# Kernel optimization log

Hardware: AMD Instinct MI355X
Metric: run time of the kernel (lower is better)

Reference implementation:

```python
import jax, jax.numpy as jnp
import numpy as np

B, CIN, COUT, L, K, HEADS, GROUPS, EPS = 16, 256, 512, 1024, 3, 8, 32, 1e-5


def group_norm(x, w, b, groups, eps=EPS):
    Bx, C, Lx = x.shape
    g = x.reshape(Bx, groups, C // groups, Lx)
    mu = g.mean(axis=(2, 3), keepdims=True)
    var = g.var(axis=(2, 3), keepdims=True)
    g = (g - mu) * jax.lax.rsqrt(var + eps)
    return g.reshape(Bx, C, Lx) * w[None, :, None] + b[None, :, None]


def conv1d(x, w, b, pad):
    y = jax.lax.conv_general_dilated(x, w, window_strides=(1,), padding=[(pad, pad)],
                                     dimension_numbers=('NCH', 'OIH', 'NCH'))
    return y + b[None, :, None]


def setup_inputs() -> dict:
    key = jax.random.key(0)
    ks = jax.random.split(key, 12)
    def kn(k, shape, fan_in, scale=1.0):
        return (np.sqrt(1.0 / fan_in) * jax.random.normal(k, shape, dtype=jnp.float32)) * scale
    return {
        'x': jax.random.normal(ks[0], (B, CIN, L), dtype=jnp.float32),
        'norm0_w': jnp.ones((CIN,), jnp.float32), 'norm0_b': jnp.zeros((CIN,), jnp.float32),
        'conv0_w': kn(ks[1], (COUT, CIN, K), CIN * K), 'conv0_b': jnp.zeros((COUT,), jnp.float32),
        'norm1_w': jnp.ones((COUT,), jnp.float32), 'norm1_b': jnp.zeros((COUT,), jnp.float32),
        'conv1_w': kn(ks[2], (COUT, COUT, K), COUT * K, 1e-5), 'conv1_b': jnp.zeros((COUT,), jnp.float32),
        'skip_w': kn(ks[3], (COUT, CIN, 1), CIN), 'skip_b': jnp.zeros((COUT,), jnp.float32),
        'norm2_w': jnp.ones((COUT,), jnp.float32), 'norm2_b': jnp.zeros((COUT,), jnp.float32),
        'qkv_w': kn(ks[4], (COUT * 3, COUT, 1), COUT), 'qkv_b': jnp.zeros((COUT * 3,), jnp.float32),
        'proj_w': kn(ks[5], (COUT, COUT, 1), COUT, 1e-5), 'proj_b': jnp.zeros((COUT,), jnp.float32),
    }


def reference(x, norm0_w, norm0_b, conv0_w, conv0_b, norm1_w, norm1_b, conv1_w, conv1_b,
              skip_w, skip_b, norm2_w, norm2_b, qkv_w, qkv_b, proj_w, proj_b):
    orig = x
    h = conv1d(jax.nn.silu(group_norm(x, norm0_w, norm0_b, min(GROUPS, CIN))), conv0_w, conv0_b, (K - 1) // 2)
    h = jax.nn.silu(group_norm(h, norm1_w, norm1_b, min(GROUPS, COUT)))
    h = conv1d(h, conv1_w, conv1_b, (K - 1) // 2)
    h = h + conv1d(orig, skip_w, skip_b, 0)  # skip (in != out), dropout p=0
    # skip_scale = 1
    # attention: qkv [B, 3C, L] -> [B*H, C/H, 3, L] (channel axis splits as H, C/H, 3)
    qkv = conv1d(group_norm(h, norm2_w, norm2_b, min(GROUPS, COUT)), qkv_w, qkv_b, 0)
    ch = COUT // HEADS
    qkv = qkv.reshape(B * HEADS, ch, 3, L)
    q, k, v = qkv[:, :, 0], qkv[:, :, 1], qkv[:, :, 2]  # each [BH, ch, L]
    scores = jnp.einsum('nci,ncj->nij', q, k) / np.sqrt(ch).astype(np.float32)
    attn = jax.nn.softmax(scores, axis=-1)
    a = jnp.einsum('nij,ncj->nci', attn, v).reshape(B, COUT, L)
    return h + conv1d(a, proj_w, proj_b, 0)
```

## Files before the change

### kernel.cpp

```cpp
#include <hip/hip_runtime.h>


typedef float f32x4 __attribute__((ext_vector_type(4)));
typedef float f32x16 __attribute__((ext_vector_type(16)));
typedef short short8 __attribute__((ext_vector_type(8)));

__device__ __forceinline__ unsigned short f2bf(float f) {
  union { float f; unsigned u; } v; v.f = f;
  return (unsigned short)((v.u + 0x7FFFu + ((v.u >> 16) & 1u)) >> 16);
}

__device__ __forceinline__ void gload_lds16(const void* g, void* l) {
  __builtin_amdgcn_global_load_lds(
      (const __attribute__((address_space(1))) unsigned int*)g,
      (__attribute__((address_space(3))) unsigned int*)l, 16, 0, 0);
}

__device__ __forceinline__ float swap_add(float x) {
  float a = x, b = x;
  asm("v_permlane32_swap_b32 %0, %1" : "+v"(a), "+v"(b));
  return a + b;
}

__device__ __forceinline__ short8 pack8(float a0, float a1, float a2, float a3,
                                        float a4, float a5, float a6, float a7) {
  unsigned x0, x1, x2, x3;
  asm("v_cvt_pk_bf16_f32 %0, %1, %2" : "=v"(x0) : "v"(a0), "v"(a1));
  asm("v_cvt_pk_bf16_f32 %0, %1, %2" : "=v"(x1) : "v"(a2), "v"(a3));
  asm("v_cvt_pk_bf16_f32 %0, %1, %2" : "=v"(x2) : "v"(a4), "v"(a5));
  asm("v_cvt_pk_bf16_f32 %0, %1, %2" : "=v"(x3) : "v"(a6), "v"(a7));
  asm("v_permlane32_swap_b32 %0, %1" : "+v"(x0), "+v"(x2));
  asm("v_permlane32_swap_b32 %0, %1" : "+v"(x1), "+v"(x3));
  union { unsigned u[4]; short8 s; } r;
  r.u[0] = x0; r.u[1] = x1; r.u[2] = x2; r.u[3] = x3;
  return r.s;
}
#define PACK8(V, B) pack8(V[B+0], V[B+1], V[B+2], V[B+3], V[B+4], V[B+5], V[B+6], V[B+7])

template<int CPG>
__global__ __launch_bounds__(256) void gn_stats_kernel(
    const float* __restrict__ in, float2* __restrict__ mr,
    unsigned short* __restrict__ outT) {
  constexpr int C = CPG * 32;
  constexpr int N = CPG * 1024;
  const int g = blockIdx.x & 31;
  const int bb = blockIdx.x >> 5;
  const size_t base = ((size_t)bb * C + g * CPG) * 1024;
  const int t = threadIdx.x;
  float s = 0.f, ss = 0.f;
#pragma unroll
  for (int i = t * 4; i < N; i += 1024) {
    const float4 v = *(const float4*)(in + base + i);
    s += (v.x + v.y) + (v.z + v.w);
    ss += (v.x * v.x + v.y * v.y) + (v.z * v.z + v.w * v.w);
  }
#pragma unroll
  for (int off = 32; off; off >>= 1) {
    s += __shfl_down(s, off);
    ss += __shfl_down(ss, off);
  }
  __shared__ float2 red[4];
  if ((t & 63) == 0) red[t >> 6] = make_float2(s, ss);
  __syncthreads();
  const float2 r0 = red[0], r1 = red[1], r2 = red[2], r3 = red[3];
  const float tots = (r0.x + r1.x) + (r2.x + r3.x);
  const float totss = (r0.y + r1.y) + (r2.y + r3.y);
  constexpr float inv_n = 1.0f / (float)N;
  const float mean = tots * inv_n;
  const float var = totss * inv_n - mean * mean;
  const float rstd = rsqrtf(var + 1e-5f);
  if (t == 0) mr[bb * 32 + g] = make_float2(mean, rstd);
  unsigned short* ob = outT + (size_t)bb * 1026 * C + g * CPG;
  if (t < CPG) {
    ob[t] = 0;
    ob[(size_t)1025 * C + t] = 0;
  }
}

template<int MODE, bool SILU, int C, bool PADZ>
__global__ __launch_bounds__(256) void nt_kernel(
    const float* __restrict__ in, const float2* __restrict__ st,
    const float* __restrict__ gw, const float* __restrict__ gb,
    unsigned short* __restrict__ outT) {
  constexpr int CPG = C / 32;
  __shared__ float ls[64][65];
  __shared__ float2 gstat[4];
  const int b = blockIdx.z, c0 = blockIdx.y * 64, l0 = blockIdx.x * 64;
  const int t = threadIdx.x;
  if (MODE == 2) {
    if (t < 4) {
      const int g = (c0 >> 4) + t;
      const float2* p = st + (((size_t)b * 4 + (g >> 3)) * 8 + (g & 7)) * 8;
      float s = 0.f, ss = 0.f;
#pragma unroll
      for (int i = 0; i < 8; ++i) { s += p[i].x; ss += p[i].y; }
      const float mean = s * (1.f / 16384.f);
      const float var = ss * (1.f / 16384.f) - mean * mean;
      gstat[t] = make_float2(mean, rsqrtf(var + 1e-5f));
    }
    __syncthreads();
  }
  const int lw = (t & 15) * 4;
  const int cr = t >> 4;
#pragma unroll
  for (int p = 0; p < 4; ++p) {
    const int c = p * 16 + cr;
    const int cc = c0 + c;
    float sc = 1.f, bi = 0.f;
    if (MODE == 1) {
      const float2 ms = st[b * 32 + cc / CPG];
      sc = gw[cc] * ms.y;
      bi = gb[cc] - ms.x * sc;
    } else if (MODE == 2) {
      const float2 ms = gstat[c >> 4];
      sc = gw[cc] * ms.y;
      bi = gb[cc] - ms.x * sc;
    }
    const float4 v = *(const float4*)(in + ((size_t)b * C + cc) * 1024 + l0 + lw);
    float o[4] = {v.x * sc + bi, v.y * sc + bi, v.z * sc + bi, v.w * sc + bi};
    if (SILU) {
#pragma unroll
      for (int d = 0; d < 4; ++d) o[d] = o[d] / (1.f + __expf(-o[d]));
    }
#pragma unroll
    for (int d = 0; d < 4; ++d) ls[c][lw + d] = o[d];
  }
  __syncthreads();
  const int l = t >> 2, c16 = (t & 3) * 16;
  short8 v0, v1;
#pragma unroll
  for (int j = 0; j < 8; ++j) v0[j] = (short)f2bf(ls[c16 + j][l]);
#pragma unroll
  for (int j = 0; j < 8; ++j) v1[j] = (short)f2bf(ls[c16 + 8 + j][l]);
  unsigned short* ob = outT + ((size_t)b * 1026 + l0 + l + 1) * C + c0 + c16;
  *(short8*)ob = v0;
  *(short8*)(ob + 8) = v1;
  if (PADZ) {
    const short8 z = {};
    if (blockIdx.x == 0 && t < 8)
      *(short8*)(outT + (size_t)b * 1026 * C + c0 + t * 8) = z;
    if (blockIdx.x == 15 && t < 8)
      *(short8*)(outT + ((size_t)b * 1026 + 1025) * C + c0 + t * 8) = z;
  }
}

__global__ void prep_w3(const float* __restrict__ w, unsigned short* __restrict__ o,
                        int Cout, int Cin) {
  const int idx = blockIdx.x * 256 + threadIdx.x;
  if (idx >= Cout * Cin * 3) return;
  const int ci = idx % Cin;
  const int rem = idx / Cin;
  const int co = rem % Cout;
  const int kk = rem / Cout;
  o[idx] = f2bf(w[((size_t)co * Cin + ci) * 3 + kk]);
}
__global__ void prep_w1(const float* __restrict__ w, unsigned short* __restrict__ o,
                        int n) {
  const int idx = blockIdx.x * 256 + threadIdx.x;
  if (idx < n) o[idx] = f2bf(w[idx]);
}
__global__ void prep_wq(const float* __restrict__ w, unsigned short* __restrict__ o) {
  const int idx = blockIdx.x * 256 + threadIdx.x;
  if (idx >= 1536 * 512) return;
  const int ci = idx & 511;
  const int m = idx >> 9;
  const int s = m >> 9, rem = m & 511, h = rem >> 6, c = rem & 63;
  o[idx] = f2bf(w[((size_t)(h * 192 + c * 3 + s) * 512) + ci]);
}

template<int K, bool ADD, bool SCATTER, bool FUSE, bool STATS>
__global__ __launch_bounds__(256, 2) void convmm_kernel(
    const unsigned short* __restrict__ Xt, const unsigned short* __restrict__ Wt,
    const float* __restrict__ bias, const float* __restrict__ addsrc,
    float* __restrict__ outp,
    unsigned short* __restrict__ qd, unsigned short* __restrict__ kd,
    unsigned short* __restrict__ vd, int Cin, int Cout,
    const unsigned short* __restrict__ X2, const unsigned short* __restrict__ W2,
    const float* __restrict__ bias2, int Cin2, float2* __restrict__ part) {
  constexpr int XR = (K == 3) ? 160 : 128;
  __shared__ __align__(16) unsigned short smem[K * 128 * 64 + XR * 64];
  unsigned short* wT = smem;
  unsigned short* xT = smem + K * 128 * 64;
  const int t = threadIdx.x, lane = t & 63, w = t >> 6;
  const int b = blockIdx.z, co0 = blockIdx.y * 128, l0 = blockIdx.x * 128;
  const int m0 = (w >> 1) * 64, n0 = (w & 1) * 64;
  const int START = (K == 3) ? l0 : (l0 + 1);
  f32x4 acc[4][4] = {};
  for (int ci0 = 0; ci0 < Cin; ci0 += 64) {
    __syncthreads();
    for (int rr = 0; rr < K * 4; ++rr) {
      const int row = rr * 32 + (t >> 3);
      const int co = row & 127;
      const int c16 = (t & 7) ^ (co & 7);
      gload_lds16(Wt + ((size_t)(row >> 7) * Cout + co0 + co) * Cin + ci0 + c16 * 8,
                  (char*)wT + (rr * 256 + t) * 16);
    }
    for (int rr = 0; rr < XR / 32; ++rr) {
      const int r = rr * 32 + (t >> 3);
      int lp = START + r;
      if (lp > 1025) lp = 1025;
      const int c16 = (t & 7) ^ (r & 7);
      gload_lds16(Xt + ((size_t)b * 1026 + lp) * Cin + ci0 + c16 * 8,
                  (char*)xT + (rr * 256 + t) * 16);
    }
    __syncthreads();
#pragma unroll
    for (int kk = 0; kk < K; ++kk) {
#pragma unroll
      for (int ks = 0; ks < 2; ++ks) {
        short8 af[4], bfr[4];
#pragma unroll
        for (int mf = 0; mf < 4; ++mf) {
          const int row = m0 + mf * 16 + (lane & 15);
          const int u = (kk * 128 + row) * 8 + ((ks * 4 + (lane >> 4)) ^ (row & 7));
          af[mf] = *(const short8*)(wT + u * 8);
        }
#pragma unroll
        for (int nf = 0; nf < 4; ++nf) {
          const int r = n0 + nf * 16 + (lane & 15) + kk;
          const int u = r * 8 + ((ks * 4 + (lane >> 4)) ^ (r & 7));
          bfr[nf] = *(const short8*)(xT + u * 8);
        }
#pragma unroll
        for (int mf = 0; mf < 4; ++mf)
#pragma unroll
          for (int nf = 0; nf < 4; ++nf)
            acc[mf][nf] = __builtin_amdgcn_mfma_f32_16x16x32_bf16(
                af[mf], bfr[nf], acc[mf][nf], 0, 0, 0);
      }
    }
  }
  if (FUSE) {
    for (int ci0 = 0; ci0 < Cin2; ci0 += 64) {
      __syncthreads();
      for (int rr = 0; rr < 4; ++rr) {
        const int co = rr * 32 + (t >> 3);
        const int c16 = (t & 7) ^ (co & 7);
        gload_lds16(W2 + (size_t)(co0 + co) * Cin2 + ci0 + c16 * 8,
                    (char*)wT + (rr * 256 + t) * 16);
      }
      for (int rr = 0; rr < 4; ++rr) {
        const int r = rr * 32 + (t >> 3);
        const int lp = l0 + 1 + r;
        const int c16 = (t & 7) ^ (r & 7);
        gload_lds16(X2 + ((size_t)b * 1026 + lp) * Cin2 + ci0 + c16 * 8,
                    (char*)xT + (rr * 256 + t) * 16);
      }
      __syncthreads();
#pragma unroll
      for (int ks = 0; ks < 2; ++ks) {
        short8 af[4], bfr[4];
#pragma unroll
        for (int mf = 0; mf < 4; ++mf) {
          const int row = m0 + mf * 16 + (lane & 15);
          const int u = row * 8 + ((ks * 4 + (lane >> 4)) ^ (row & 7));
          af[mf] = *(const short8*)(wT + u * 8);
        }
#pragma unroll
        for (int nf = 0; nf < 4; ++nf) {
          const int r = n0 + nf * 16 + (lane & 15);
          const int u = r * 8 + ((ks * 4 + (lane >> 4)) ^ (r & 7));
          bfr[nf] = *(const short8*)(xT + u * 8);
        }
#pragma unroll
        for (int mf = 0; mf < 4; ++mf)
#pragma unroll
          for (int nf = 0; nf < 4; ++nf)
            acc[mf][nf] = __builtin_amdgcn_mfma_f32_16x16x32_bf16(
                af[mf], bfr[nf], acc[mf][nf], 0, 0, 0);
      }
    }
  }
  if (!SCATTER) {
    float sg[4] = {}, ssg[4] = {};
#pragma unroll
    for (int mf = 0; mf < 4; ++mf) {
#pragma unroll
      for (int r = 0; r < 4; ++r) {
        const int co = co0 + m0 + mf * 16 + (lane >> 4) * 4 + r;
        float bv = bias[co];
        if (FUSE) bv += bias2[co];
#pragma unroll
        for (int nf = 0; nf < 4; ++nf) {
          const int l = l0 + n0 + nf * 16 + (lane & 15);
          const size_t o = ((size_t)b * Cout + co) * 1024 + l;
          float v = acc[mf][nf][r] + bv;
          if (ADD) v += addsrc[o];
          outp[o] = v;
          if (STATS) { sg[mf] += v; ssg[mf] += v * v; }
        }
      }
    }
    if (STATS) {
      __syncthreads();
      float2* sr = (float2*)smem;
#pragma unroll
      for (int mf = 0; mf < 4; ++mf) {
        float s = sg[mf], ss = ssg[mf];
#pragma unroll
        for (int off = 32; off; off >>= 1) {
          s += __shfl_down(s, off);
          ss += __shfl_down(ss, off);
        }
        if (lane == 0)
          sr[(((w >> 1) * 4 + mf) << 1) | (w & 1)] = make_float2(s, ss);
      }
      __syncthreads();
      if (t < 8) {
        const float2 a = sr[t * 2], c = sr[t * 2 + 1];
        part[(((size_t)b * 4 + blockIdx.y) * 8 + t) * 8 + blockIdx.x] =
            make_float2(a.x + c.x, a.y + c.y);
      }
    }
  } else {
    __syncthreads();
    unsigned short* TP = smem;
    const int sidx = co0 >> 9;
    const int mbase = co0 & 511;
    const float qscale = (sidx == 0) ? 0.18033688f : 1.0f;
    if (sidx < 2) {
#pragma unroll
      for (int mf = 0; mf < 4; ++mf)
#pragma unroll
        for (int r = 0; r < 4; ++r) {
          const int mloc = m0 + mf * 16 + (lane >> 4) * 4 + r;
          const int mg = mbase + mloc;
          const float bv = bias[(mg >> 6) * 192 + (mg & 63) * 3 + sidx];
#pragma unroll
          for (int nf = 0; nf < 4; ++nf) {
            const int l = n0 + nf * 16 + (lane & 15);
            const int u = l * 16 + ((mloc >> 3) ^ (l & 7));
            TP[u * 8 + (mloc & 7)] = f2bf((acc[mf][nf][r] + bv) * qscale);
          }
        }
      __syncthreads();
      unsigned short* dst = (sidx == 0) ? qd : kd;
      for (int it = 0; it < 8; ++it) {
        const int idx = it * 256 + t;
        const int l = idx >> 4, mu = idx & 15;
        const int mg = mbase + mu * 8;
        const int bh = b * 8 + (mg >> 6);
        const short8 v = *(const short8*)(TP + (l * 16 + (mu ^ (l & 7))) * 8);
        *(short8*)(dst + ((size_t)bh * 1024 + l0 + l) * 64 + (mg & 63)) = v;
      }
    } else {
#pragma unroll
      for (int mf = 0; mf < 4; ++mf)
#pragma unroll
        for (int r = 0; r < 4; ++r) {
          const int mloc = m0 + mf * 16 + (lane >> 4) * 4 + r;
          const int mg = mbase + mloc;
          const float bv = bias[(mg >> 6) * 192 + (mg & 63) * 3 + 2];
#pragma unroll
          for (int nf = 0; nf < 4; ++nf) {
            const int l = n0 + nf * 16 + (lane & 15);
            const int u = mloc * 16 + ((l >> 3) ^ ((mloc & 7) << 1));
            TP[u * 8 + (l & 7)] = f2bf(acc[mf][nf][r] + bv);
          }
        }
      __syncthreads();
      for (int it = 0; it < 8; ++it) {
        const int idx = it * 256 + t;
        const int mloc = idx >> 4, lu = idx & 15;
        const int mg = mbase + mloc;
        const int bh = b * 8 + (mg >> 6);
        const short8 v =
            *(const short8*)(TP + (mloc * 16 + (lu ^ ((mloc & 7) << 1))) * 8);
        *(short8*)(vd + ((size_t)bh * 64 + (mg & 63)) * 1024 + l0 + lu * 8) = v;
      }
    }
  }
}

__global__ __launch_bounds__(256, 4) void attn_mfma(
    const unsigned short* __restrict__ Qb, const unsigned short* __restrict__ Kb,
    const unsigned short* __restrict__ Vb, unsigned short* __restrict__ Ab) {
  __shared__ __align__(16) unsigned short Ks[2][64 * 64];
  __shared__ __align__(16) unsigned short Vs[2][64 * 64];
  unsigned short* QP = &Ks[0][0];
  const int t = threadIdx.x, lane = t & 63, w = t >> 6;
  const int hi = lane >> 5, l31 = lane & 31;
  const int id = blockIdx.x;
  const int slot = id >> 3;
  const int bh = ((id & 7) << 4) | (slot >> 3);
  const int b = bh >> 3, h = bh & 7;
  const int iq0 = (slot & 7) * 128;
  const unsigned short* Qg = Qb + ((size_t)bh * 1024 + iq0) * 64;
  const unsigned short* Kg = Kb + (size_t)bh * 1024 * 64;
  const unsigned short* Vg = Vb + (size_t)bh * 64 * 1024;
  for (int rr = 0; rr < 4; ++rr) {
    const int r = rr * 32 + (t >> 3), c16 = (t & 7) ^ (r & 7);
    gload_lds16(Qg + (size_t)r * 64 + c16 * 8, (char*)QP + (rr * 256 + t) * 16);
  }
  __syncthreads();
  const int irow = w * 32 + l31;
  short8 qf[4];
#pragma unroll
  for (int kc = 0; kc < 4; ++kc) {
    const int u = irow * 8 + ((kc * 2 + hi) ^ (irow & 7));
    qf[kc] = *(const short8*)(QP + u * 8);
  }
  __syncthreads();
  for (int rr = 0; rr < 2; ++rr) {
    const int r = rr * 32 + (t >> 3), c16 = (t & 7) ^ (r & 7);
    gload_lds16(Kg + (size_t)r * 64 + c16 * 8, (char*)Ks[0] + (rr * 256 + t) * 16);
    gload_lds16(Vg + (size_t)r * 1024 + c16 * 8, (char*)Vs[0] + (rr * 256 + t) * 16);
  }
  __syncthreads();
  float l = 0.f;
  f32x16 oA[2] = {};
  for (int ti = 0; ti < 16; ++ti) {
    const int cur = ti & 1;
    if (ti < 15) {
      const int j1 = (ti + 1) * 64;
      for (int rr = 0; rr < 2; ++rr) {
        const int r = rr * 32 + (t >> 3), c16 = (t & 7) ^ (r & 7);
        gload_lds16(Kg + (size_t)(j1 + r) * 64 + c16 * 8,
                    (char*)Ks[cur ^ 1] + (rr * 256 + t) * 16);
        gload_lds16(Vg + (size_t)r * 1024 + j1 + c16 * 8,
                    (char*)Vs[cur ^ 1] + (rr * 256 + t) * 16);
      }
    }
    f32x16 sA0 = {}, sA1 = {};
    __builtin_amdgcn_s_setprio(1);
#pragma unroll
    for (int kc = 0; kc < 4; ++kc) {
      const int r0 = l31, r1 = 32 + l31;
      const short8 k0 = *(const short8*)(Ks[cur] + (r0 * 8 + ((kc * 2 + hi) ^ (r0 & 7))) * 8);
      const short8 k1 = *(const short8*)(Ks[cur] + (r1 * 8 + ((kc * 2 + hi) ^ (r1 & 7))) * 8);
      sA0 = __builtin_amdgcn_mfma_f32_32x32x16_bf16(k0, qf[kc], sA0, 0, 0, 0);
      sA1 = __builtin_amdgcn_mfma_f32_32x32x16_bf16(k1, qf[kc], sA1, 0, 0, 0);
    }
    __builtin_amdgcn_s_setprio(0);
    float p0 = 0.f, p1 = 0.f, p2 = 0.f, p3 = 0.f;
#pragma unroll
    for (int r = 0; r < 16; r += 4) {
      sA0[r + 0] = exp2f(sA0[r + 0]); p0 += sA0[r + 0];
      sA0[r + 1] = exp2f(sA0[r + 1]); p1 += sA0[r + 1];
      sA0[r + 2] = exp2f(sA0[r + 2]); p2 += sA0[r + 2];
      sA0[r + 3] = exp2f(sA0[r + 3]); p3 += sA0[r + 3];
    }
#pragma unroll
    for (int r = 0; r < 16; r += 4) {
      sA1[r + 0] = exp2f(sA1[r + 0]); p0 += sA1[r + 0];
      sA1[r + 1] = exp2f(sA1[r + 1]); p1 += sA1[r + 1];
      sA1[r + 2] = exp2f(sA1[r + 2]); p2 += sA1[r + 2];
      sA1[r + 3] = exp2f(sA1[r + 3]); p3 += sA1[r + 3];
    }
    l += (p0 + p1) + (p2 + p3);
    short8 pb[4];
    pb[0] = PACK8(sA0, 0);
    pb[1] = PACK8(sA0, 8);
    pb[2] = PACK8(sA1, 0);
    pb[3] = PACK8(sA1, 8);
    __builtin_amdgcn_s_setprio(1);
#pragma unroll
    for (int cf = 0; cf < 2; ++cf) {
      const int row = cf * 32 + l31;
#pragma unroll
      for (int s = 0; s < 4; ++s) {
        const int u = row * 8 + ((s * 2 + hi) ^ (row & 7));
        const short8 va = *(const short8*)(Vs[cur] + u * 8);
        oA[cf] = __builtin_amdgcn_mfma_f32_32x32x16_bf16(va, pb[s], oA[cf], 0, 0, 0);
      }
    }
    __builtin_amdgcn_s_setprio(0);
    __syncthreads();
  }
  const float inv = 1.f / swap_add(l);
#pragma unroll
  for (int cf = 0; cf < 2; ++cf)
#pragma unroll
    for (int r = 0; r < 16; ++r) {
      const int c = cf * 32 + (r & 3) + 8 * (r >> 2) + 4 * hi;
      const int u = irow * 8 + ((c >> 3) ^ (irow & 7));
      QP[u * 8 + (c & 7)] = f2bf(oA[cf][r] * inv);
    }
  for (int rr = 0; rr < 4; ++rr) {
    const int row = w * 32 + rr * 8 + (lane >> 3);
    const int c16 = lane & 7;
    const int u = row * 8 + (c16 ^ (row & 7));
    const short8 vv = *(const short8*)(QP + u * 8);
    *(short8*)(Ab + ((size_t)b * 1026 + iq0 + row + 1) * 512 + h * 64 + c16 * 8) = vv;
  }
}

#define MB(x) ((size_t)(x) << 20)

extern "C" void kernel_launch(void* const* d_in, const int* in_sizes, int n_in,
                              void* d_out, int out_size, void* d_ws,
                              size_t ws_size, hipStream_t stream) {
  const float* x   = (const float*)d_in[0];
  const float* n0w = (const float*)d_in[1];
  const float* n0b = (const float*)d_in[2];
  const float* c0w = (const float*)d_in[3];
  const float* c0b = (const float*)d_in[4];
  const float* n1w = (const float*)d_in[5];
  const float* n1b = (const float*)d_in[6];
  const float* c1w = (const float*)d_in[7];
  const float* c1b = (const float*)d_in[8];
  const float* skw = (const float*)d_in[9];
  const float* skb = (const float*)d_in[10];
  const float* n2w = (const float*)d_in[11];
  const float* n2b = (const float*)d_in[12];
  const float* qw  = (const float*)d_in[13];
  const float* qb  = (const float*)d_in[14];
  const float* pw  = (const float*)d_in[15];
  const float* pb  = (const float*)d_in[16];
  char* wsb = (char*)d_ws;
  unsigned short* WT0 = (unsigned short*)(wsb);
  unsigned short* WT1 = (unsigned short*)(wsb + MB(1));
  unsigned short* WSK = (unsigned short*)(wsb + MB(3));
  unsigned short* WQ  = (unsigned short*)(wsb + MB(4));
  unsigned short* WP  = (unsigned short*)(wsb + MB(6));
  float* H2           = (float*)(wsb + MB(7));
  unsigned short* Qb2 = (unsigned short*)(wsb + MB(41));
  unsigned short* Kb2 = (unsigned short*)(wsb + MB(58));
  float* H0           = (float*)(wsb + MB(75));
  unsigned short* Vb2 = (unsigned short*)(wsb + MB(75));
  unsigned short* Xt2 = (unsigned short*)(wsb + MB(92));
  unsigned short* Xt0 = (unsigned short*)(wsb + MB(109));
  unsigned short* Xt1 = (unsigned short*)(wsb + MB(109));
  unsigned short* Ab  = (unsigned short*)(wsb + MB(109));
  unsigned short* Xbf = (unsigned short*)(wsb + MB(126));
  float2* MR0   = (float2*)(wsb + MB(135));
  float2* PART1 = (float2*)(wsb + MB(135) + 8192);
  float2* PART2 = (float2*)(wsb + MB(135) + 32768);
  float* outp = (float*)d_out;

  prep_w3<<<1536, 256, 0, stream>>>(c0w, WT0, 512, 256);
  prep_w3<<<3072, 256, 0, stream>>>(c1w, WT1, 512, 512);
  prep_w1<<<512, 256, 0, stream>>>(skw, WSK, 512 * 256);
  prep_wq<<<3072, 256, 0, stream>>>(qw, WQ);
  prep_w1<<<1024, 256, 0, stream>>>(pw, WP, 512 * 512);

  gn_stats_kernel<8><<<512, 256, 0, stream>>>(x, MR0, Xt0);
  nt_kernel<1, true, 256, false><<<dim3(16, 4, 16), 256, 0, stream>>>(
      x, MR0, n0w, n0b, Xt0);
  convmm_kernel<3, false, false, false, true><<<dim3(8, 4, 16), 256, 0, stream>>>(
      Xt0, WT0, c0b, nullptr, H0, nullptr, nullptr, nullptr, 256, 512,
      nullptr, nullptr, nullptr, 0, PART1);
  nt_kernel<0, false, 256, false><<<dim3(16, 4, 16), 256, 0, stream>>>(
      x, nullptr, nullptr, nullptr, Xbf);
  nt_kernel<2, true, 512, true><<<dim3(16, 8, 16), 256, 0, stream>>>(
      H0, PART1, n1w, n1b, Xt1);
  convmm_kernel<3, false, false, true, true><<<dim3(8, 4, 16), 256, 0, stream>>>(
      Xt1, WT1, c1b, nullptr, H2, nullptr, nullptr, nullptr, 512, 512,
      Xbf, WSK, skb, 256, PART2);
  nt_kernel<2, false, 512, false><<<dim3(16, 8, 16), 256, 0, stream>>>(
      H2, PART2, n2w, n2b, Xt2);
  convmm_kernel<1, false, true, false, false><<<dim3(8, 12, 16), 256, 0, stream>>>(
      Xt2, WQ, qb, nullptr, nullptr, Qb2, Kb2, Vb2, 512, 1536,
      nullptr, nullptr, nullptr, 0, nullptr);
  attn_mfma<<<dim3(1024), 256, 0, stream>>>(Qb2, Kb2, Vb2, Ab);
  convmm_kernel<1, true, false, false, false><<<dim3(8, 4, 16), 256, 0, stream>>>(
      Ab, WP, pb, H2, outp, nullptr, nullptr, nullptr, 512, 512,
      nullptr, nullptr, nullptr, 0, nullptr);
}
```

Before: 212.5 us.

## Fuse weight prep, emit transposed bf16 conv0 output, merge raw-x transpose

Merges the five weight-prep launches into one kernel. Folds the raw-x bf16 transpose into the first normalize/transpose kernel. Makes conv0 write its output as transposed bf16 directly from LDS, so a lighter elementwise kernel can apply groupnorm+SiLU without another transpose. Also unrolls the attention KV loop by two via a lambda. These cut launch count and fp32 intermediate traffic, at the cost of storing conv0 output in bf16 before normalization, which adds rounding.

```diff
diff --git a/kernel.cpp b/kernel.cpp
--- a/kernel.cpp
+++ b/kernel.cpp
@@ -8,6 +8,10 @@
 __device__ __forceinline__ unsigned short f2bf(float f) {
   union { float f; unsigned u; } v; v.f = f;
   return (unsigned short)((v.u + 0x7FFFu + ((v.u >> 16) & 1u)) >> 16);
+}
+__device__ __forceinline__ float bf2f(unsigned short h) {
+  union { unsigned u; float f; } v; v.u = ((unsigned)h) << 16;
+  return v.f;
 }
 
 __device__ __forceinline__ void gload_lds16(const void* g, void* l) {
@@ -77,13 +81,14 @@
   }
 }
 
-template<int MODE, bool SILU, int C, bool PADZ>
+template<int MODE, bool SILU, int C, bool PADZ, bool RAW>
 __global__ __launch_bounds__(256) void nt_kernel(
     const float* __restrict__ in, const float2* __restrict__ st,
     const float* __restrict__ gw, const float* __restrict__ gb,
-    unsigned short* __restrict__ outT) {
+    unsigned short* __restrict__ outT, unsigned short* __restrict__ rawT) {
   constexpr int CPG = C / 32;
   __shared__ float ls[64][65];
+  __shared__ unsigned short lsr[RAW ? 64 : 1][72];
   __shared__ float2 gstat[4];
   const int b = blockIdx.z, c0 = blockIdx.y * 64, l0 = blockIdx.x * 64;
   const int t = threadIdx.x;
@@ -117,6 +122,12 @@
       bi = gb[cc] - ms.x * sc;
     }
     const float4 v = *(const float4*)(in + ((size_t)b * C + cc) * 1024 + l0 + lw);
+    if (RAW) {
+      lsr[c][lw + 0] = f2bf(v.x);
+      lsr[c][lw + 1] = f2bf(v.y);
+      lsr[c][lw + 2] = f2bf(v.z);
+      lsr[c][lw + 3] = f2bf(v.w);
+    }
     float o[4] = {v.x * sc + bi, v.y * sc + bi, v.z * sc + bi, v.w * sc + bi};
     if (SILU) {
 #pragma unroll
@@ -135,6 +146,16 @@
   unsigned short* ob = outT + ((size_t)b * 1026 + l0 + l + 1) * C + c0 + c16;
   *(short8*)ob = v0;
   *(short8*)(ob + 8) = v1;
+  if (RAW) {
+    short8 w0, w1;
+#pragma unroll
+    for (int j = 0; j < 8; ++j) w0[j] = (short)lsr[c16 + j][l];
+#pragma unroll
+    for (int j = 0; j < 8; ++j) w1[j] = (short)lsr[c16 + 8 + j][l];
+    unsigned short* rb = rawT + ((size_t)b * 1026 + l0 + l + 1) * C + c0 + c16;
+    *(short8*)rb = w0;
+    *(short8*)(rb + 8) = w1;
+  }
   if (PADZ) {
     const short8 z = {};
     if (blockIdx.x == 0 && t < 8)
@@ -144,31 +165,88 @@
   }
 }
 
-__global__ void prep_w3(const float* __restrict__ w, unsigned short* __restrict__ o,
-                        int Cout, int Cin) {
-  const int idx = blockIdx.x * 256 + threadIdx.x;
-  if (idx >= Cout * Cin * 3) return;
-  const int ci = idx % Cin;
-  const int rem = idx / Cin;
-  const int co = rem % Cout;
-  const int kk = rem / Cout;
-  o[idx] = f2bf(w[((size_t)co * Cin + ci) * 3 + kk]);
-}
-__global__ void prep_w1(const float* __restrict__ w, unsigned short* __restrict__ o,
-                        int n) {
-  const int idx = blockIdx.x * 256 + threadIdx.x;
-  if (idx < n) o[idx] = f2bf(w[idx]);
-}
-__global__ void prep_wq(const float* __restrict__ w, unsigned short* __restrict__ o) {
-  const int idx = blockIdx.x * 256 + threadIdx.x;
-  if (idx >= 1536 * 512) return;
-  const int ci = idx & 511;
-  const int m = idx >> 9;
-  const int s = m >> 9, rem = m & 511, h = rem >> 6, c = rem & 63;
-  o[idx] = f2bf(w[((size_t)(h * 192 + c * 3 + s) * 512) + ci]);
-}
-
-template<int K, bool ADD, bool SCATTER, bool FUSE, bool STATS>
+__global__ __launch_bounds__(256) void ntE_kernel(
+    const unsigned short* __restrict__ Ht, const float2* __restrict__ part,
+    const float* __restrict__ gw, const float* __restrict__ gb,
+    unsigned short* __restrict__ outT) {
+  __shared__ float2 gstat[32];
+  const int b = blockIdx.y;
+  const int t = threadIdx.x;
+  if (t < 32) {
+    const float2* p = part + (((size_t)b * 4 + (t >> 3)) * 8 + (t & 7)) * 8;
+    float s = 0.f, ss = 0.f;
+#pragma unroll
+    for (int i = 0; i < 8; ++i) { s += p[i].x; ss += p[i].y; }
+    const float mean = s * (1.f / 16384.f);
+    const float var = ss * (1.f / 16384.f) - mean * mean;
+    gstat[t] = make_float2(mean, rsqrtf(var + 1e-5f));
+  }
+  __syncthreads();
+  const int c8 = t & 63;
+  const float2 ms = gstat[c8 >> 1];
+  const int cbase = c8 * 8;
+  const float4 g0 = *(const float4*)(gw + cbase);
+  const float4 g1 = *(const float4*)(gw + cbase + 4);
+  const float4 b0 = *(const float4*)(gb + cbase);
+  const float4 b1 = *(const float4*)(gb + cbase + 4);
+  float sc[8], bi[8];
+  sc[0] = g0.x * ms.y; sc[1] = g0.y * ms.y; sc[2] = g0.z * ms.y; sc[3] = g0.w * ms.y;
+  sc[4] = g1.x * ms.y; sc[5] = g1.y * ms.y; sc[6] = g1.z * ms.y; sc[7] = g1.w * ms.y;
+  bi[0] = b0.x - ms.x * sc[0]; bi[1] = b0.y - ms.x * sc[1];
+  bi[2] = b0.z - ms.x * sc[2]; bi[3] = b0.w - ms.x * sc[3];
+  bi[4] = b1.x - ms.x * sc[4]; bi[5] = b1.y - ms.x * sc[5];
+  bi[6] = b1.z - ms.x * sc[6]; bi[7] = b1.w - ms.x * sc[7];
+#pragma unroll
+  for (int pass = 0; pass < 4; ++pass) {
+    const int lp = blockIdx.x * 16 + pass * 4 + (t >> 6) + 1;
+    const size_t o = ((size_t)b * 1026 + lp) * 512 + cbase;
+    const short8 v = *(const short8*)(Ht + o);
+    short8 r;
+#pragma unroll
+    for (int e = 0; e < 8; ++e) {
+      const float y = bf2f((unsigned short)v[e]) * sc[e] + bi[e];
+      r[e] = (short)f2bf(y / (1.f + __expf(-y)));
+    }
+    *(short8*)(outT + o) = r;
+  }
+  const short8 z = {};
+  if (blockIdx.x == 0 && t < 64)
+    *(short8*)(outT + (size_t)b * 1026 * 512 + t * 8) = z;
+  if (blockIdx.x == 63 && t < 64)
+    *(short8*)(outT + ((size_t)b * 1026 + 1025) * 512 + t * 8) = z;
+}
+
+__global__ void prep_all(const float* __restrict__ c0w, const float* __restrict__ c1w,
+                         const float* __restrict__ skw, const float* __restrict__ qw,
+                         const float* __restrict__ pw,
+                         unsigned short* __restrict__ WT0, unsigned short* __restrict__ WT1,
+                         unsigned short* __restrict__ WSK, unsigned short* __restrict__ WQ,
+                         unsigned short* __restrict__ WP) {
+  int idx = blockIdx.x * 256 + threadIdx.x;
+  if (idx < 393216) {
+    const int ci = idx & 255; const int rem = idx >> 8;
+    const int co = rem & 511; const int kk = rem >> 9;
+    WT0[idx] = f2bf(c0w[((size_t)co * 256 + ci) * 3 + kk]); return;
+  }
+  idx -= 393216;
+  if (idx < 786432) {
+    const int ci = idx & 511; const int rem = idx >> 9;
+    const int co = rem & 511; const int kk = rem >> 9;
+    WT1[idx] = f2bf(c1w[((size_t)co * 512 + ci) * 3 + kk]); return;
+  }
+  idx -= 786432;
+  if (idx < 131072) { WSK[idx] = f2bf(skw[idx]); return; }
+  idx -= 131072;
+  if (idx < 786432) {
+    const int ci = idx & 511; const int m = idx >> 9;
+    const int s = m >> 9, rem = m & 511, h = rem >> 6, c = rem & 63;
+    WQ[idx] = f2bf(qw[((size_t)(h * 192 + c * 3 + s) * 512) + ci]); return;
+  }
+  idx -= 786432;
+  WP[idx] = f2bf(pw[idx]);
+}
+
+template<int K, bool ADD, bool SCATTER, bool FUSE, bool STATS, bool TROUT>
 __global__ __launch_bounds__(256, 2) void convmm_kernel(
     const unsigned short* __restrict__ Xt, const unsigned short* __restrict__ Wt,
     const float* __restrict__ bias, const float* __restrict__ addsrc,
@@ -271,7 +349,50 @@
       }
     }
   }
-  if (!SCATTER) {
+  if (TROUT) {
+    __syncthreads();
+    unsigned short* TP = smem;
+    float2* sr = (float2*)(TP + 128 * 128);
+    float sg[4] = {}, ssg[4] = {};
+#pragma unroll
+    for (int mf = 0; mf < 4; ++mf)
+#pragma unroll
+      for (int r = 0; r < 4; ++r) {
+        const int mloc = m0 + mf * 16 + (lane >> 4) * 4 + r;
+        const float bv = bias[co0 + mloc];
+#pragma unroll
+        for (int nf = 0; nf < 4; ++nf) {
+          const int l = n0 + nf * 16 + (lane & 15);
+          const float v = acc[mf][nf][r] + bv;
+          sg[mf] += v; ssg[mf] += v * v;
+          const int u = l * 16 + ((mloc >> 3) ^ (l & 7));
+          TP[u * 8 + (mloc & 7)] = f2bf(v);
+        }
+      }
+#pragma unroll
+    for (int mf = 0; mf < 4; ++mf) {
+      float s = sg[mf], ss = ssg[mf];
+#pragma unroll
+      for (int off = 32; off; off >>= 1) {
+        s += __shfl_down(s, off);
+        ss += __shfl_down(ss, off);
+      }
+      if (lane == 0)
+        sr[(((w >> 1) * 4 + mf) << 1) | (w & 1)] = make_float2(s, ss);
+    }
+    __syncthreads();
+    for (int it = 0; it < 8; ++it) {
+      const int idx = it * 256 + t;
+      const int l = idx >> 4, mu = idx & 15;
+      const short8 v = *(const short8*)(TP + (l * 16 + (mu ^ (l & 7))) * 8);
+      *(short8*)(qd + ((size_t)b * 1026 + l0 + l + 1) * 512 + co0 + mu * 8) = v;
+    }
+    if (t < 8) {
+      const float2 a = sr[t * 2], c = sr[t * 2 + 1];
+      part[(((size_t)b * 4 + blockIdx.y) * 8 + t) * 8 + blockIdx.x] =
+          make_float2(a.x + c.x, a.y + c.y);
+    }
+  } else if (!SCATTER) {
     float sg[4] = {}, ssg[4] = {};
 #pragma unroll
     for (int mf = 0; mf < 4; ++mf) {
@@ -407,10 +528,9 @@
     gload_lds16(Vg + (size_t)r * 1024 + c16 * 8, (char*)Vs[0] + (rr * 256 + t) * 16);
   }
   __syncthreads();
-  float l = 0.f;
+  float lsum = 0.f;
   f32x16 oA[2] = {};
-  for (int ti = 0; ti < 16; ++ti) {
-    const int cur = ti & 1;
+  auto kv_iter = [&](const int ti, const int cur) {
     if (ti < 15) {
       const int j1 = (ti + 1) * 64;
       for (int rr = 0; rr < 2; ++rr) {
@@ -447,7 +567,7 @@
       sA1[r + 2] = exp2f(sA1[r + 2]); p2 += sA1[r + 2];
       sA1[r + 3] = exp2f(sA1[r + 3]); p3 += sA1[r + 3];
     }
-    l += (p0 + p1) + (p2 + p3);
+    lsum += (p0 + p1) + (p2 + p3);
     short8 pb[4];
     pb[0] = PACK8(sA0, 0);
     pb[1] = PACK8(sA0, 8);
@@ -466,8 +586,12 @@
     }
     __builtin_amdgcn_s_setprio(0);
     __syncthreads();
-  }
-  const float inv = 1.f / swap_add(l);
+  };
+  for (int ti = 0; ti < 16; ti += 2) {
+    kv_iter(ti, 0);
+    kv_iter(ti + 1, 1);
+  }
+  const float inv = 1.f / swap_add(lsum);
 #pragma unroll
   for (int cf = 0; cf < 2; ++cf)
 #pragma unroll
@@ -516,7 +640,7 @@
   float* H2           = (float*)(wsb + MB(7));
   unsigned short* Qb2 = (unsigned short*)(wsb + MB(41));
   unsigned short* Kb2 = (unsigned short*)(wsb + MB(58));
-  float* H0           = (float*)(wsb + MB(75));
+  unsigned short* H0t = (unsigned short*)(wsb + MB(75));
   unsigned short* Vb2 = (unsigned short*)(wsb + MB(75));
   unsigned short* Xt2 = (unsigned short*)(wsb + MB(92));
   unsigned short* Xt0 = (unsigned short*)(wsb + MB(109));
@@ -528,32 +652,25 @@
   float2* PART2 = (float2*)(wsb + MB(135) + 32768);
   float* outp = (float*)d_out;
 
-  prep_w3<<<1536, 256, 0, stream>>>(c0w, WT0, 512, 256);
-  prep_w3<<<3072, 256, 0, stream>>>(c1w, WT1, 512, 512);
-  prep_w1<<<512, 256, 0, stream>>>(skw, WSK, 512 * 256);
-  prep_wq<<<3072, 256, 0, stream>>>(qw, WQ);
-  prep_w1<<<1024, 256, 0, stream>>>(pw, WP, 512 * 512);
+  prep_all<<<9216, 256, 0, stream>>>(c0w, c1w, skw, qw, pw, WT0, WT1, WSK, WQ, WP);
 
   gn_stats_kernel<8><<<512, 256, 0, stream>>>(x, MR0, Xt0);
-  nt_kernel<1, true, 256, false><<<dim3(16, 4, 16), 256, 0, stream>>>(
-      x, MR0, n0w, n0b, Xt0);
-  convmm_kernel<3, false, false, false, true><<<dim3(8, 4, 16), 256, 0, stream>>>(
-      Xt0, WT0, c0b, nullptr, H0, nullptr, nullptr, nullptr, 256, 512,
+  nt_kernel<1, true, 256, false, true><<<dim3(16, 4, 16), 256, 0, stream>>>(
+      x, MR0, n0w, n0b, Xt0, Xbf);
+  convmm_kernel<3, false, false, false, true, true><<<dim3(8, 4, 16), 256, 0, stream>>>(
+      Xt0, WT0, c0b, nullptr, nullptr, H0t, nullptr, nullptr, 256, 512,
       nullptr, nullptr, nullptr, 0, PART1);
-  nt_kernel<0, false, 256, false><<<dim3(16, 4, 16), 256, 0, stream>>>(
-      x, nullptr, nullptr, nullptr, Xbf);
-  nt_kernel<2, true, 512, true><<<dim3(16, 8, 16), 256, 0, stream>>>(
-      H0, PART1, n1w, n1b, Xt1);
-  convmm_kernel<3, false, false, true, true><<<dim3(8, 4, 16), 256, 0, stream>>>(
+  ntE_kernel<<<dim3(64, 16), 256, 0, stream>>>(H0t, PART1, n1w, n1b, Xt1);
+  convmm_kernel<3, false, false, true, true, false><<<dim3(8, 4, 16), 256, 0, stream>>>(
       Xt1, WT1, c1b, nullptr, H2, nullptr, nullptr, nullptr, 512, 512,
       Xbf, WSK, skb, 256, PART2);
-  nt_kernel<2, false, 512, false><<<dim3(16, 8, 16), 256, 0, stream>>>(
-      H2, PART2, n2w, n2b, Xt2);
-  convmm_kernel<1, false, true, false, false><<<dim3(8, 12, 16), 256, 0, stream>>>(
+  nt_kernel<2, false, 512, false, false><<<dim3(16, 8, 16), 256, 0, stream>>>(
+      H2, PART2, n2w, n2b, Xt2, nullptr);
+  convmm_kernel<1, false, true, false, false, false><<<dim3(8, 12, 16), 256, 0, stream>>>(
       Xt2, WQ, qb, nullptr, nullptr, Qb2, Kb2, Vb2, 512, 1536,
       nullptr, nullptr, nullptr, 0, nullptr);
   attn_mfma<<<dim3(1024), 256, 0, stream>>>(Qb2, Kb2, Vb2, Ab);
-  convmm_kernel<1, true, false, false, false><<<dim3(8, 4, 16), 256, 0, stream>>>(
+  convmm_kernel<1, true, false, false, false, false><<<dim3(8, 4, 16), 256, 0, stream>>>(
       Ab, WP, pb, H2, outp, nullptr, nullptr, nullptr, 512, 512,
       nullptr, nullptr, nullptr, 0, nullptr);
 }
```

Result: faster. 199.2 us (-6.3%).
